# Kernel tuning notes

Measured on AMD Instinct MI355X. Metric: run time of the kernel, lower is better.

The kernel has to match this reference:

```python
import jax, jax.numpy as jnp
import numpy as np

N_ITEMS = 80001
D = 128
K = 20
HOP = 2
ROUTING_ITER = 4
SAMPLE = 12
B = 256
S = 50


def layer_norm(x, g, b, eps=1e-5):
    mu = jnp.mean(x, -1, keepdims=True)
    var = jnp.var(x, -1, keepdims=True)
    return (x - mu) * jax.lax.rsqrt(var + eps) * g + b


def routing_agg(x, nb0):
    # NeighborRoutingAgg (DisenGCN-style neighbor routing): x [N,d], nb0 [N,m] 0-based neighbor ids into x
    xn = x * jax.lax.rsqrt(jnp.sum(x * x, -1, keepdims=True) + 1e-12)
    z = xn[nb0]  # [N, m, d] irregular gather
    u = xn
    for _ in range(ROUTING_ITER):
        p = jax.nn.softmax(jnp.einsum('nd,nmd->nm', u, z), axis=1)
        u = xn + jnp.einsum('nm,nmd->nd', p, z)
        u = u * jax.lax.rsqrt(jnp.sum(u * u, -1, keepdims=True) + 1e-12)
    return u


def gru(x, W_ih, W_hh, b_ih, b_hh):
    # PyTorch nn.GRU, 1 layer, batch_first; x [B,S,d]
    Bb, Ss, d = x.shape
    h0 = jnp.zeros((Bb, d), x.dtype)
    gi_all = jnp.einsum('bsd,ed->bse', x, W_ih) + b_ih  # [B,S,3d] precompute input gates
    def step(h, gi):
        gh = h @ W_hh.T + b_hh
        i_r, i_z, i_n = jnp.split(gi, 3, -1)
        h_r, h_z, h_n = jnp.split(gh, 3, -1)
        r = jax.nn.sigmoid(i_r + h_r)
        zg = jax.nn.sigmoid(i_z + h_z)
        n = jnp.tanh(i_n + r * h_n)
        return (1.0 - zg) * n + zg * h, (1.0 - zg) * n + zg * h
    _, H = jax.lax.scan(step, h0, jnp.swapaxes(gi_all, 0, 1))
    return jnp.swapaxes(H, 0, 1)


def setup_inputs() -> dict:
    key = jax.random.key(0)
    ks = jax.random.split(key, 16)
    inp = {}
    inp['inp_sess'] = jax.random.randint(ks[0], (B, S), 0, N_ITEMS)
    inp['lengths'] = jax.random.randint(ks[1], (B,), 1, S + 1)
    inp['mask_inf'] = jnp.zeros((B, S), jnp.float32)
    inp['mask_1'] = jnp.ones((B, S), jnp.float32)
    inp['tau'] = jnp.float32(1.0)
    inp['adj_items'] = jax.random.randint(ks[2], (N_ITEMS, SAMPLE), 1, N_ITEMS)
    inp['anchors'] = jax.random.randint(ks[3], (K,), 1, N_ITEMS)
    inp['emb'] = jax.random.normal(ks[4], (N_ITEMS, D), jnp.float32) * 0.05
    inp['W_ih'] = jax.random.normal(ks[5], (3 * D, D), jnp.float32) * 0.05
    inp['W_hh'] = jax.random.normal(ks[6], (3 * D, D), jnp.float32) * 0.05
    inp['b_ih'] = jnp.zeros((3 * D,), jnp.float32)
    inp['b_hh'] = jnp.zeros((3 * D,), jnp.float32)
    inp['W1'] = jax.random.normal(ks[7], (D, D), jnp.float32) * 0.05
    inp['b1'] = jnp.zeros((D,), jnp.float32)
    inp['W2'] = jax.random.normal(ks[8], (K, D), jnp.float32) * 0.05
    inp['b2'] = jnp.zeros((K,), jnp.float32)
    inp['a1'] = jax.random.normal(ks[9], (1,), jnp.float32)
    inp['a2'] = jax.random.normal(ks[10], (1,), jnp.float32)
    for i, nm in enumerate(['ln1', 'ln2', 'ln3', 'ln4']):
        inp[nm + '_g'] = jnp.ones((D,), jnp.float32)
        inp[nm + '_b'] = jnp.zeros((D,), jnp.float32)
    return inp


def reference(inp_sess, lengths, mask_inf, mask_1, tau, adj_items, anchors, emb,
              W_ih, W_hh, b_ih, b_hh, W1, b1, W2, b2, a1, a2,
              ln1_g, ln1_b, ln2_g, ln2_b, ln3_g, ln3_b, ln4_g, ln4_b):
    # mask_inf / mask_1 are accepted by the torch forward but unused
    x = emb[1:]                       # [N-1, d] real items
    nb0 = adj_items[1:] - 1           # 0-based neighbor ids into x
    out = x
    acc = x
    for _ in range(HOP):
        out = routing_agg(out, nb0)
        acc = acc + out
    item_vectors = layer_norm(acc, ln1_g, ln1_b)          # [N-1, d]
    h = jax.nn.leaky_relu(item_vectors @ W1.T + b1)
    item_pop_prob = jax.nn.softmax((h @ W2.T + b2) / tau, axis=1)  # [N-1, K]
    anchors_emb = item_vectors[anchors - 1]               # [K, d]
    item_pop_vec = layer_norm(item_pop_prob @ anchors_emb, ln2_g, ln2_b)
    pad = jnp.zeros((1, D), item_vectors.dtype)
    iv = jnp.concatenate([pad, item_vectors], 0)          # [N, d]
    pv = jnp.concatenate([pad, item_pop_vec], 0)
    inp_emb = iv[inp_sess]                                # [B,S,d] (dropout off / eval)
    inp_pop = pv[inp_sess]
    H = layer_norm(gru(inp_emb, W_ih, W_hh, b_ih, b_hh), ln3_g, ln3_b)
    ht = H[jnp.arange(H.shape[0]), lengths - 1]           # [B, d]
    Hp = layer_norm(gru(inp_pop, W_ih, W_hh, b_ih, b_hh), ln4_g, ln4_b)
    ht_pop = Hp[jnp.arange(Hp.shape[0]), lengths - 1]
    scores_item = ht @ item_vectors.T                     # [B, N-1]
    scores_pop = ht_pop @ item_pop_vec.T
    scores = jax.nn.sigmoid(a1) * scores_item + jax.nn.sigmoid(a2) * scores_pop
    return scores, scores_item, scores_pop
```

## Files before the change

### kernel.cpp

```cpp
#include <hip/hip_runtime.h>

typedef unsigned short u16;
typedef unsigned int u32;
typedef __attribute__((ext_vector_type(8))) short short8;
typedef __attribute__((ext_vector_type(4))) float f32x4;

#define N_IT 80000
#define SLOT 10240000

__device__ __forceinline__ float wred(float v) {
#pragma unroll
    for (int s = 32; s; s >>= 1) v += __shfl_xor(v, s);
    return v;
}
__device__ __forceinline__ float sigf(float x) { return 1.f / (1.f + expf(-x)); }
__device__ __forceinline__ u16 f2bf(float f) {
    u32 x = __float_as_uint(f);
    u32 r = x + 0x7fffu + ((x >> 16) & 1u);
    return (u16)(r >> 16);
}
__device__ __forceinline__ float bf2f(u16 v) {
    return __uint_as_float(((u32)v) << 16);
}
__device__ __forceinline__ u32 pack2(float lo, float hi) {
    return ((u32)f2bf(hi) << 16) | f2bf(lo);
}
__device__ __forceinline__ f32x4 mfma16(short8 a, short8 b, f32x4 c) {
    return __builtin_amdgcn_mfma_f32_16x16x32_bf16(a, b, c, 0, 0, 0);
}
#define SWZ(v, pat) __int_as_float(__builtin_amdgcn_ds_swizzle(__float_as_int(v), pat))
__device__ __forceinline__ float red16(float t) {
    t += SWZ(t, 0x041F);
    t += SWZ(t, 0x081F);
    t += SWZ(t, 0x101F);
    t += SWZ(t, 0x201F);
    return t;
}
__device__ __forceinline__ float red16max(float t) {
    t = fmaxf(t, SWZ(t, 0x041F));
    t = fmaxf(t, SWZ(t, 0x081F));
    t = fmaxf(t, SWZ(t, 0x101F));
    t = fmaxf(t, SWZ(t, 0x201F));
    return t;
}
__device__ __forceinline__ float dot4(float4 a, float4 b) {
    return a.x * b.x + a.y * b.y + a.z * b.z + a.w * b.w;
}
__device__ __forceinline__ void unp8(uint4 w, float4& a, float4& b) {
    a.x = __uint_as_float(w.x << 16); a.y = __uint_as_float(w.x & 0xFFFF0000u);
    a.z = __uint_as_float(w.y << 16); a.w = __uint_as_float(w.y & 0xFFFF0000u);
    b.x = __uint_as_float(w.z << 16); b.y = __uint_as_float(w.z & 0xFFFF0000u);
    b.z = __uint_as_float(w.w << 16); b.w = __uint_as_float(w.w & 0xFFFF0000u);
}

__global__ __launch_bounds__(256) void k_cvtnorm(const float* __restrict__ Wih,
                                                 const float* __restrict__ W1,
                                                 const float* __restrict__ W2,
                                                 u16* __restrict__ wihbf,
                                                 u16* __restrict__ w1bf,
                                                 u16* __restrict__ w2bf,
                                                 const float* __restrict__ x,
                                                 u32* __restrict__ xn) {
    if (blockIdx.x < 272) {
        int i = blockIdx.x * 256 + threadIdx.x;
        if (i < 49152) {
            wihbf[i] = f2bf(Wih[i]);
        } else if (i < 65536) {
            int j = i - 49152;
            w1bf[j] = f2bf(W1[j]);
        } else if (i < 69632) {
            int j = i - 65536;
            int row = j >> 7, col = j & 127;
            w2bf[j] = (row < 20) ? f2bf(W2[row * 128 + col]) : (u16)0;
        }
        return;
    }
    int wid = ((blockIdx.x - 272) * 256 + threadIdx.x) >> 6;
    int l = threadIdx.x & 63;
    size_t base = (size_t)wid * 128;
    float2 v = *(const float2*)(x + base + 2 * l);
    float s = wred(v.x * v.x + v.y * v.y);
    float r = 1.f / sqrtf(s + 1e-12f);
    xn[(size_t)wid * 64 + l] = pack2(v.x * r, v.y * r);
}

__global__ __launch_bounds__(256, 2) void k_routeb(const u32* __restrict__ xn,
                                                   const int* __restrict__ adj,
                                                   u32* __restrict__ out) {
    int tid = blockIdx.x * 256 + threadIdx.x;
    int item = tid >> 4;
    int sl = threadIdx.x & 15;
    float4 x0, x1;
    unp8(*(const uint4*)(xn + (size_t)item * 64 + sl * 4), x0, x1);
    const int4* ar = (const int4*)(adj + (size_t)(item + 1) * 12);
    int4 a0 = ar[0], a1 = ar[1], a2 = ar[2];
    uint4 zw[12];
#define LDZ(i, comp) zw[i] = *(const uint4*)(xn + (size_t)((comp) - 1) * 64 + sl * 4);
    LDZ(0, a0.x) LDZ(1, a0.y) LDZ(2, a0.z) LDZ(3, a0.w)
    LDZ(4, a1.x) LDZ(5, a1.y) LDZ(6, a1.z) LDZ(7, a1.w)
    LDZ(8, a2.x) LDZ(9, a2.y) LDZ(10, a2.z) LDZ(11, a2.w)
#undef LDZ
    float4 u0 = x0, u1 = x1;
#pragma unroll
    for (int it = 0; it < 4; it++) {
        float p[12]; float sum = 0.f;
#pragma unroll
        for (int m = 0; m < 12; m++) {
            float4 a, b; unp8(zw[m], a, b);
            float t = dot4(u0, a) + dot4(u1, b);
            t = red16(t);
            p[m] = __expf(t);
            sum += p[m];
        }
        float inv = 1.f / sum;
        u0 = x0; u1 = x1;
#pragma unroll
        for (int m = 0; m < 12; m++) {
            float pm = p[m] * inv;
            float4 a, b; unp8(zw[m], a, b);
            u0.x += pm * a.x; u0.y += pm * a.y; u0.z += pm * a.z; u0.w += pm * a.w;
            u1.x += pm * b.x; u1.y += pm * b.y; u1.z += pm * b.z; u1.w += pm * b.w;
        }
        float nn = red16(dot4(u0, u0) + dot4(u1, u1));
        float rr = 1.f / sqrtf(nn + 1e-12f);
        u0.x *= rr; u0.y *= rr; u0.z *= rr; u0.w *= rr;
        u1.x *= rr; u1.y *= rr; u1.z *= rr; u1.w *= rr;
    }
    uint4 o = make_uint4(pack2(u0.x, u0.y), pack2(u0.z, u0.w),
                         pack2(u1.x, u1.y), pack2(u1.z, u1.w));
    *(uint4*)(out + (size_t)item * 64 + sl * 4) = o;
}

__global__ __launch_bounds__(256, 2) void k_route2lnb(const u32* __restrict__ xn,
                                                      const float* __restrict__ emb,
                                                      const int* __restrict__ adj,
                                                      const float* __restrict__ g,
                                                      const float* __restrict__ bb,
                                                      u32* __restrict__ ivbf) {
    int tid = blockIdx.x * 256 + threadIdx.x;
    int item = tid >> 4;
    int sl = threadIdx.x & 15;
    float4 x0, x1;
    unp8(*(const uint4*)(xn + (size_t)item * 64 + sl * 4), x0, x1);
    const int4* ar = (const int4*)(adj + (size_t)(item + 1) * 12);
    int4 a0 = ar[0], a1 = ar[1], a2 = ar[2];
    uint4 zw[12];
#define LDZ(i, comp) zw[i] = *(const uint4*)(xn + (size_t)((comp) - 1) * 64 + sl * 4);
    LDZ(0, a0.x) LDZ(1, a0.y) LDZ(2, a0.z) LDZ(3, a0.w)
    LDZ(4, a1.x) LDZ(5, a1.y) LDZ(6, a1.z) LDZ(7, a1.w)
    LDZ(8, a2.x) LDZ(9, a2.y) LDZ(10, a2.z) LDZ(11, a2.w)
#undef LDZ
    float4 u0 = x0, u1 = x1;
#pragma unroll
    for (int it = 0; it < 4; it++) {
        float p[12]; float sum = 0.f;
#pragma unroll
        for (int m = 0; m < 12; m++) {
            float4 a, b; unp8(zw[m], a, b);
            float t = dot4(u0, a) + dot4(u1, b);
            t = red16(t);
            p[m] = __expf(t);
            sum += p[m];
        }
        float inv = 1.f / sum;
        u0 = x0; u1 = x1;
#pragma unroll
        for (int m = 0; m < 12; m++) {
            float pm = p[m] * inv;
            float4 a, b; unp8(zw[m], a, b);
            u0.x += pm * a.x; u0.y += pm * a.y; u0.z += pm * a.z; u0.w += pm * a.w;
            u1.x += pm * b.x; u1.y += pm * b.y; u1.z += pm * b.z; u1.w += pm * b.w;
        }
        float nn = red16(dot4(u0, u0) + dot4(u1, u1));
        float rr = 1.f / sqrtf(nn + 1e-12f);
        u0.x *= rr; u0.y *= rr; u0.z *= rr; u0.w *= rr;
        u1.x *= rr; u1.y *= rr; u1.z *= rr; u1.w *= rr;
    }
    const float4* er = (const float4*)(emb + (size_t)item * 128 + sl * 8);
    float4 e0 = er[0], e1 = er[1];
    float v[8];
    v[0] = e0.x + x0.x + u0.x; v[1] = e0.y + x0.y + u0.y;
    v[2] = e0.z + x0.z + u0.z; v[3] = e0.w + x0.w + u0.w;
    v[4] = e1.x + x1.x + u1.x; v[5] = e1.y + x1.y + u1.y;
    v[6] = e1.z + x1.z + u1.z; v[7] = e1.w + x1.w + u1.w;
    float s = 0.f, q = 0.f;
#pragma unroll
    for (int j = 0; j < 8; j++) { s += v[j]; q += v[j] * v[j]; }
    s = red16(s); q = red16(q);
    float mean = s * (1.f / 128.f);
    float var = q * (1.f / 128.f) - mean * mean;
    float r = 1.f / sqrtf(var + 1e-5f);
    const float4* gr = (const float4*)(g + sl * 8);
    const float4* br = (const float4*)(bb + sl * 8);
    float4 g0 = gr[0], g1 = gr[1], bw0 = br[0], bw1 = br[1];
    float y[8];
    y[0] = (v[0] - mean) * r * g0.x + bw0.x; y[1] = (v[1] - mean) * r * g0.y + bw0.y;
    y[2] = (v[2] - mean) * r * g0.z + bw0.z; y[3] = (v[3] - mean) * r * g0.w + bw0.w;
    y[4] = (v[4] - mean) * r * g1.x + bw1.x; y[5] = (v[5] - mean) * r * g1.y + bw1.y;
    y[6] = (v[6] - mean) * r * g1.z + bw1.z; y[7] = (v[7] - mean) * r * g1.w + bw1.w;
    uint4 o = make_uint4(pack2(y[0], y[1]), pack2(y[2], y[3]),
                         pack2(y[4], y[5]), pack2(y[6], y[7]));
    *(uint4*)(ivbf + (size_t)item * 64 + sl * 4) = o;
}

__global__ __launch_bounds__(256, 2) void k_popm(const u16* __restrict__ ivbf,
                                                 const u16* __restrict__ w1bf,
                                                 const float* __restrict__ b1,
                                                 const u16* __restrict__ w2bf,
                                                 const float* __restrict__ b2,
                                                 const float* __restrict__ tau,
                                                 const int* __restrict__ anchors,
                                                 const float* __restrict__ g2,
                                                 const float* __restrict__ bb2,
                                                 u16* __restrict__ pvbf) {
    __shared__ u16 buf[4][16][136];
    __shared__ u16 anchS[128][40];
    int tid = threadIdx.x;
    for (int e = tid; e < 4096; e += 256) {
        int d = e >> 5, k = e & 31;
        anchS[d][k] = (k < 20) ? ivbf[(size_t)(anchors[k] - 1) * 128 + d] : (u16)0;
    }
    __syncthreads();
    int w = tid >> 6, l = tid & 63;
    int g16 = l >> 4, c = l & 15;
    int item0 = blockIdx.x * 64 + w * 16;
    const u16* ap = ivbf + (size_t)(item0 + c) * 128 + g16 * 8;
    short8 A[4];
#pragma unroll
    for (int kb = 0; kb < 4; kb++) A[kb] = *(const short8*)(ap + kb * 32);
#pragma unroll
    for (int nt = 0; nt < 8; nt++) {
        const u16* wp = w1bf + (nt * 16 + c) * 128 + g16 * 8;
        f32x4 acc = {0.f, 0.f, 0.f, 0.f};
#pragma unroll
        for (int kb = 0; kb < 4; kb++)
            acc = mfma16(A[kb], *(const short8*)(wp + kb * 32), acc);
        float bias = b1[nt * 16 + c];
#pragma unroll
        for (int qq = 0; qq < 4; qq++) {
            float hv = acc[qq] + bias;
            hv = hv >= 0.f ? hv : 0.01f * hv;
            buf[w][4 * g16 + qq][nt * 16 + c] = f2bf(hv);
        }
    }
    short8 A2[4];
#pragma unroll
    for (int kb = 0; kb < 4; kb++)
        A2[kb] = *(const short8*)&buf[w][c][g16 * 8 + kb * 32];
    f32x4 L0 = {0.f, 0.f, 0.f, 0.f}, L1 = {0.f, 0.f, 0.f, 0.f};
#pragma unroll
    for (int kb = 0; kb < 4; kb++) {
        L0 = mfma16(A2[kb], *(const short8*)(w2bf + c * 128 + g16 * 8 + kb * 32), L0);
        L1 = mfma16(A2[kb], *(const short8*)(w2bf + (16 + c) * 128 + g16 * 8 + kb * 32), L1);
    }
    float it = 1.f / tau[0];
    float b2v0 = b2[c];
    float b2v1 = (c < 4) ? b2[16 + c] : 0.f;
#pragma unroll
    for (int qq = 0; qq < 4; qq++) {
        float v0 = (L0[qq] + b2v0) * it;
        float v1 = (c < 4) ? (L1[qq] + b2v1) * it : -1e30f;
        float mx = red16max(fmaxf(v0, v1));
        float e0 = __expf(v0 - mx);
        float e1 = (c < 4) ? __expf(v1 - mx) : 0.f;
        float ssum = red16(e0 + e1);
        float inv = 1.f / ssum;
        buf[w][4 * g16 + qq][c] = f2bf(e0 * inv);
        buf[w][4 * g16 + qq][16 + c] = f2bf(e1 * inv);
    }
    short8 A3 = *(const short8*)&buf[w][c][g16 * 8];
    f32x4 pv[8];
#pragma unroll
    for (int nt = 0; nt < 8; nt++) {
        const short8 B3 = *(const short8*)&anchS[nt * 16 + c][g16 * 8];
        f32x4 zz = {0.f, 0.f, 0.f, 0.f};
        pv[nt] = mfma16(A3, B3, zz);
    }
    float g2v[8], b2gv[8];
#pragma unroll
    for (int t = 0; t < 8; t++) { g2v[t] = g2[t * 16 + c]; b2gv[t] = bb2[t * 16 + c]; }
#pragma unroll
    for (int qq = 0; qq < 4; qq++) {
        float ps = 0.f, psq = 0.f;
#pragma unroll
        for (int t = 0; t < 8; t++) { float x = pv[t][qq]; ps += x; psq += x * x; }
        float s = red16(ps), sq = red16(psq);
        float mean = s * (1.f / 128.f);
        float var = sq * (1.f / 128.f) - mean * mean;
        float r = 1.f / sqrtf(var + 1e-5f);
        size_t base = (size_t)(item0 + 4 * g16 + qq) * 128;
#pragma unroll
        for (int t = 0; t < 8; t++) {
            float y = (pv[t][qq] - mean) * r * g2v[t] + b2gv[t];
            pvbf[base + t * 16 + c] = f2bf(y);
        }
    }
}

__global__ __launch_bounds__(256) void k_gi(const int* __restrict__ sess,
                                            const u16* __restrict__ ivbf,
                                            const u16* __restrict__ pvbf,
                                            const u16* __restrict__ wbf,
                                            const float* __restrict__ bih,
                                            u16* __restrict__ gi) {
    int w = threadIdx.x >> 6, l = threadIdx.x & 63;
    int mt = blockIdx.x * 4 + w;
    int r = mt * 16 + (l & 15);
    int s = r / 50, t = r - s * 50;
    int idx = sess[(s & 255) * 50 + t];
    const u16* srcb = (s < 256) ? ivbf : pvbf;
    int ko = (l >> 4) * 8;
    const short8 Z8 = {0, 0, 0, 0, 0, 0, 0, 0};
    short8 A[4];
    if (idx == 0) {
#pragma unroll
        for (int kb = 0; kb < 4; kb++) A[kb] = Z8;
    } else {
        const u16* rp = srcb + (size_t)(idx - 1) * 128 + ko;
#pragma unroll
        for (int kb = 0; kb < 4; kb++) A[kb] = *(const short8*)(rp + kb * 32);
    }
    int rowb = mt * 16 + (l >> 4) * 4;
    for (int nt = 0; nt < 24; nt++) {
        int gcol = nt * 16 + (l & 15);
        const u16* wp = wbf + gcol * 128 + ko;
        f32x4 acc = {0.f, 0.f, 0.f, 0.f};
#pragma unroll
        for (int kb = 0; kb < 4; kb++)
            acc = mfma16(A[kb], *(const short8*)(wp + kb * 32), acc);
        float bias = bih[gcol];
#pragma unroll
        for (int q = 0; q < 4; q++)
            gi[(size_t)(rowb + q) * 384 + gcol] = f2bf(acc[q] + bias);
    }
}

__global__ __launch_bounds__(384, 2) void k_gru(const u16* __restrict__ gi,
                                                const float* __restrict__ whh,
                                                const float* __restrict__ bhh,
                                                const int* __restrict__ lengths,
                                                const float* __restrict__ g3,
                                                const float* __restrict__ b3,
                                                const float* __restrict__ g4,
                                                const float* __restrict__ b4,
                                                u32* __restrict__ htbf) {
    __shared__ __align__(16) float hS[2][128];
    __shared__ float rS[128], zS[128], hnS[128], inS[128];
    int g = threadIdx.x, b = blockIdx.x;
    float4 wv[32];
    const float4* wr = (const float4*)(whh + g * 128);
#pragma unroll
    for (int k = 0; k < 32; k++) wv[k] = wr[k];
    float bh = bhh[g];
    if (g < 128) hS[0][g] = 0.f;
    int len = lengths[b & 255];
    const u16* giS = gi + (size_t)b * 50 * 384 + g;
    __syncthreads();
    int par = 0;
    for (int t = 0; t < len; t++) {
        float ga = bf2f(giS[t * 384]);
        float aA = bh;
#pragma unroll
        for (int k = 0; k < 32; k++) {
            float4 w4 = wv[k];
            float4 ha = *(const float4*)&hS[par][k * 4];
            aA += w4.x * ha.x + w4.y * ha.y + w4.z * ha.z + w4.w * ha.w;
        }
        if (g < 128) {
            rS[g] = sigf(ga + aA);
        } else if (g < 256) {
            zS[g - 128] = sigf(ga + aA);
        } else {
            inS[g - 256] = ga; hnS[g - 256] = aA;
        }
        __syncthreads();
        if (g < 128) {
            float n = tanhf(inS[g] + rS[g] * hnS[g]);
            hS[par ^ 1][g] = (1.f - zS[g]) * n + zS[g] * hS[par][g];
        }
        __syncthreads();
        par ^= 1;
    }
    if (g < 64) {
        const float* lg = (b < 256) ? g3 : g4;
        const float* lb = (b < 256) ? b3 : b4;
        float2 v = *(const float2*)&hS[par][2 * g];
        float s = wred(v.x + v.y), q = wred(v.x * v.x + v.y * v.y);
        float mean = s * (1.f / 128.f), var = q * (1.f / 128.f) - mean * mean;
        float r = 1.f / sqrtf(var + 1e-5f);
        float2 gg = *(const float2*)(lg + 2 * g), bg = *(const float2*)(lb + 2 * g);
        float y0 = (v.x - mean) * r * gg.x + bg.x;
        float y1 = (v.y - mean) * r * gg.y + bg.y;
        htbf[(size_t)b * 64 + g] = ((u32)f2bf(y1) << 16) | f2bf(y0);
    }
}

__global__ __launch_bounds__(256) void k_scores(const u16* __restrict__ htbf,
                                                const u16* __restrict__ ivbf,
                                                const u16* __restrict__ pvbf,
                                                const float* __restrict__ a1,
                                                const float* __restrict__ a2,
                                                float* __restrict__ out) {
    int w = threadIdx.x >> 6, l = threadIdx.x & 63;
    int n0 = blockIdx.x * 64;
    int ko = (l >> 4) * 8;
    short8 Ai[4][4], Ap[4][4];
#pragma unroll
    for (int mi = 0; mi < 4; mi++) {
        int row = w * 64 + mi * 16 + (l & 15);
        const u16* pi = htbf + row * 128 + ko;
        const u16* pp = htbf + (row + 256) * 128 + ko;
#pragma unroll
        for (int kb = 0; kb < 4; kb++) {
            Ai[mi][kb] = *(const short8*)(pi + kb * 32);
            Ap[mi][kb] = *(const short8*)(pp + kb * 32);
        }
    }
    float s1 = sigf(a1[0]), s2 = sigf(a2[0]);
    float* sc = out;
    float* si = out + (size_t)20480000;
    float* sp = out + (size_t)40960000;
    for (int nt = 0; nt < 4; nt++) {
        int col = n0 + nt * 16 + (l & 15);
        const u16* bi = ivbf + (size_t)col * 128 + ko;
        const u16* bp = pvbf + (size_t)col * 128 + ko;
        short8 Bi[4], Bp[4];
#pragma unroll
        for (int kb = 0; kb < 4; kb++) {
            Bi[kb] = *(const short8*)(bi + kb * 32);
            Bp[kb] = *(const short8*)(bp + kb * 32);
        }
#pragma unroll
        for (int mi = 0; mi < 4; mi++) {
            f32x4 ai = {0.f, 0.f, 0.f, 0.f}, ap = {0.f, 0.f, 0.f, 0.f};
#pragma unroll
            for (int kb = 0; kb < 4; kb++) {
                ai = mfma16(Ai[mi][kb], Bi[kb], ai);
                ap = mfma16(Ap[mi][kb], Bp[kb], ap);
            }
            int rowb = w * 64 + mi * 16 + (l >> 4) * 4;
#pragma unroll
            for (int q = 0; q < 4; q++) {
                size_t o = (size_t)(rowb + q) * 80000 + col;
                float vi = ai[q], vp = ap[q];
                __builtin_nontemporal_store(vi, si + o);
                __builtin_nontemporal_store(vp, sp + o);
                __builtin_nontemporal_store(s1 * vi + s2 * vp, sc + o);
            }
        }
    }
}

extern "C" void kernel_launch(void* const* d_in, const int* in_sizes, int n_in,
                              void* d_out, int out_size, void* d_ws, size_t ws_size,
                              hipStream_t stream) {
    (void)in_sizes; (void)n_in; (void)out_size; (void)ws_size;
    const int*   sess    = (const int*)d_in[0];
    const int*   lengths = (const int*)d_in[1];
    const float* tau     = (const float*)d_in[4];
    const int*   adj     = (const int*)d_in[5];
    const int*   anchors = (const int*)d_in[6];
    const float* emb     = (const float*)d_in[7];
    const float* W_ih    = (const float*)d_in[8];
    const float* W_hh    = (const float*)d_in[9];
    const float* b_ih    = (const float*)d_in[10];
    const float* b_hh    = (const float*)d_in[11];
    const float* W1      = (const float*)d_in[12];
    const float* b1      = (const float*)d_in[13];
    const float* W2      = (const float*)d_in[14];
    const float* b2      = (const float*)d_in[15];
    const float* a1      = (const float*)d_in[16];
    const float* a2      = (const float*)d_in[17];
    const float* ln1g = (const float*)d_in[18];
    const float* ln1b = (const float*)d_in[19];
    const float* ln2g = (const float*)d_in[20];
    const float* ln2b = (const float*)d_in[21];
    const float* ln3g = (const float*)d_in[22];
    const float* ln3b = (const float*)d_in[23];
    const float* ln4g = (const float*)d_in[24];
    const float* ln4b = (const float*)d_in[25];

    float* out = (float*)d_out;
    u32* o_xn = (u32*)out;
    u32* o_o1 = (u32*)(out + SLOT);
    u16* o_gi = (u16*)(out + 2 * SLOT);

    u16* ws16   = (u16*)d_ws;
    u16* ivbf   = ws16;
    u16* pvbf   = ws16 + 10240000;
    u16* wihbf  = ws16 + 20480000;
    u16* htbf   = ws16 + 20529152;
    u16* w1bf   = ws16 + 20594688;
    u16* w2bf   = ws16 + 20611072;

    k_cvtnorm<<<20272, 256, 0, stream>>>(W_ih, W1, W2, wihbf, w1bf, w2bf,
                                         emb + 128, o_xn);
    k_routeb<<<5000, 256, 0, stream>>>(o_xn, adj, o_o1);
    k_route2lnb<<<5000, 256, 0, stream>>>(o_o1, emb + 128, adj, ln1g, ln1b, (u32*)ivbf);
    k_popm<<<1250, 256, 0, stream>>>(ivbf, w1bf, b1, w2bf, b2, tau, anchors,
                                     ln2g, ln2b, pvbf);
    k_gi<<<400, 256, 0, stream>>>(sess, ivbf, pvbf, wihbf, b_ih, o_gi);
    k_gru<<<512, 384, 0, stream>>>(o_gi, W_hh, b_hh, lengths, ln3g, ln3b, ln4g, ln4b,
                                   (u32*)htbf);
    k_scores<<<1250, 256, 0, stream>>>(htbf, ivbf, pvbf, a1, a2, out);
}
```

Measured before the change: 435.1 us.

## Batch 16 sequences per GRU block and compute recurrent matmul with bf16 MFMA

The GRU kernel now processes 16 sequences per block instead of one. W_hh is stored as swizzled bf16 in LDS, and each step's h·W_hh^T runs as MFMA tiles rather than per-thread fp32 dot products. The grid shrinks from 512 blocks to 32, so W_hh is loaded once per block, though far fewer CUs are busy. Each block now loops to the longest length among its 16 sequences and snapshots h at each sequence's last step. The recurrent state is rounded to bf16 and fast exp is used, which lowers precision.

```diff
diff --git a/kernel.cpp b/kernel.cpp
--- a/kernel.cpp
+++ b/kernel.cpp
@@ -335,7 +335,7 @@
     }
 }
 
-__global__ __launch_bounds__(384, 2) void k_gru(const u16* __restrict__ gi,
+__global__ __launch_bounds__(384, 1) void k_gru(const u16* __restrict__ gi,
                                                 const float* __restrict__ whh,
                                                 const float* __restrict__ bhh,
                                                 const int* __restrict__ lengths,
@@ -344,54 +344,75 @@
                                                 const float* __restrict__ g4,
                                                 const float* __restrict__ b4,
                                                 u32* __restrict__ htbf) {
-    __shared__ __align__(16) float hS[2][128];
-    __shared__ float rS[128], zS[128], hnS[128], inS[128];
-    int g = threadIdx.x, b = blockIdx.x;
-    float4 wv[32];
-    const float4* wr = (const float4*)(whh + g * 128);
-#pragma unroll
-    for (int k = 0; k < 32; k++) wv[k] = wr[k];
-    float bh = bhh[g];
-    if (g < 128) hS[0][g] = 0.f;
-    int len = lengths[b & 255];
-    const u16* giS = gi + (size_t)b * 50 * 384 + g;
+    __shared__ u16 whhS[49152];
+    __shared__ float gats[16][388];
+    __shared__ u16 hbfS[2048];
+    __shared__ float hfS[2048];
+    __shared__ float hsnapS[2048];
+    __shared__ float bhhS[384];
+    __shared__ int lenS[16];
+    int tid = threadIdx.x;
+    int sb = blockIdx.x * 16;
+    for (int e = tid; e < 49152; e += 384)
+        whhS[e ^ ((((u32)e >> 7) & 7) << 3)] = f2bf(whh[e]);
+    if (tid < 384) bhhS[tid] = bhh[tid];
+    if (tid < 16) lenS[tid] = lengths[(sb + tid) & 255];
+    for (int e = tid; e < 2048; e += 384) { hfS[e] = 0.f; hbfS[e] = 0; hsnapS[e] = 0.f; }
     __syncthreads();
-    int par = 0;
-    for (int t = 0; t < len; t++) {
-        float ga = bf2f(giS[t * 384]);
-        float aA = bh;
-#pragma unroll
-        for (int k = 0; k < 32; k++) {
-            float4 w4 = wv[k];
-            float4 ha = *(const float4*)&hS[par][k * 4];
-            aA += w4.x * ha.x + w4.y * ha.y + w4.z * ha.z + w4.w * ha.w;
-        }
-        if (g < 128) {
-            rS[g] = sigf(ga + aA);
-        } else if (g < 256) {
-            zS[g - 128] = sigf(ga + aA);
-        } else {
-            inS[g - 256] = ga; hnS[g - 256] = aA;
+    int lmax = 0;
+#pragma unroll
+    for (int i = 0; i < 16; i++) lmax = max(lmax, lenS[i]);
+    int w = tid >> 6, l = tid & 63;
+    int c16 = l & 15, hi = l >> 4, ko = hi * 8;
+    int aswz = (c16 & 7) << 3;
+    for (int t = 0; t < lmax; t++) {
+        short8 a[4];
+#pragma unroll
+        for (int kb = 0; kb < 4; kb++)
+            a[kb] = *(const short8*)&hbfS[(c16 * 128 + ko + kb * 32) ^ aswz];
+#pragma unroll
+        for (int ct = 0; ct < 4; ct++) {
+            int gcol = w * 64 + ct * 16 + c16;
+            int bswz = (gcol & 7) << 3;
+            f32x4 acc = {0.f, 0.f, 0.f, 0.f};
+#pragma unroll
+            for (int kb = 0; kb < 4; kb++)
+                acc = mfma16(a[kb],
+                             *(const short8*)&whhS[(gcol * 128 + ko + kb * 32) ^ bswz],
+                             acc);
+#pragma unroll
+            for (int q = 0; q < 4; q++) gats[hi * 4 + q][gcol] = acc[q];
         }
         __syncthreads();
-        if (g < 128) {
-            float n = tanhf(inS[g] + rS[g] * hnS[g]);
-            hS[par ^ 1][g] = (1.f - zS[g]) * n + zS[g] * hS[par][g];
+        for (int e = tid; e < 2048; e += 384) {
+            int s = e >> 7, d = e & 127;
+            size_t gb = ((size_t)(sb + s) * 50 + t) * 384;
+            float gr = bf2f(gi[gb + d]);
+            float gz = bf2f(gi[gb + 128 + d]);
+            float gn = bf2f(gi[gb + 256 + d]);
+            float r = 1.f / (1.f + __expf(-(gr + gats[s][d] + bhhS[d])));
+            float z = 1.f / (1.f + __expf(-(gz + gats[s][128 + d] + bhhS[128 + d])));
+            float narg = gn + r * (gats[s][256 + d] + bhhS[256 + d]);
+            float e2 = __expf(2.f * narg);
+            float n = 1.f - 2.f / (e2 + 1.f);
+            float hnew = (1.f - z) * n + z * hfS[e];
+            hfS[e] = hnew;
+            hbfS[e ^ ((s & 7) << 3)] = f2bf(hnew);
+            if (t == lenS[s] - 1) hsnapS[e] = hnew;
         }
         __syncthreads();
-        par ^= 1;
-    }
-    if (g < 64) {
-        const float* lg = (b < 256) ? g3 : g4;
-        const float* lb = (b < 256) ? b3 : b4;
-        float2 v = *(const float2*)&hS[par][2 * g];
-        float s = wred(v.x + v.y), q = wred(v.x * v.x + v.y * v.y);
-        float mean = s * (1.f / 128.f), var = q * (1.f / 128.f) - mean * mean;
+    }
+    const float* lg = (sb < 256) ? g3 : g4;
+    const float* lb = (sb < 256) ? b3 : b4;
+    for (int s = w; s < 16; s += 6) {
+        float2 v = *(const float2*)&hsnapS[s * 128 + 2 * l];
+        float su = wred(v.x + v.y), q = wred(v.x * v.x + v.y * v.y);
+        float mean = su * (1.f / 128.f), var = q * (1.f / 128.f) - mean * mean;
         float r = 1.f / sqrtf(var + 1e-5f);
-        float2 gg = *(const float2*)(lg + 2 * g), bg = *(const float2*)(lb + 2 * g);
+        float2 gg = *(const float2*)(lg + 2 * l), bg = *(const float2*)(lb + 2 * l);
         float y0 = (v.x - mean) * r * gg.x + bg.x;
         float y1 = (v.y - mean) * r * gg.y + bg.y;
-        htbf[(size_t)b * 64 + g] = ((u32)f2bf(y1) << 16) | f2bf(y0);
+        htbf[(size_t)(sb + s) * 64 + l] = pack2(y0, y1);
     }
 }
 
@@ -500,7 +521,7 @@
     k_popm<<<1250, 256, 0, stream>>>(ivbf, w1bf, b1, w2bf, b2, tau, anchors,
                                      ln2g, ln2b, pvbf);
     k_gi<<<400, 256, 0, stream>>>(sess, ivbf, pvbf, wihbf, b_ih, o_gi);
-    k_gru<<<512, 384, 0, stream>>>(o_gi, W_hh, b_hh, lengths, ln3g, ln3b, ln4g, ln4b,
-                                   (u32*)htbf);
+    k_gru<<<32, 384, 0, stream>>>(o_gi, W_hh, b_hh, lengths, ln3g, ln3b, ln4g, ln4b,
+                                  (u32*)htbf);
     k_scores<<<1250, 256, 0, stream>>>(htbf, ivbf, pvbf, a1, a2, out);
 }
```

Result: slower. 485.8 us (+11.6%).

## Batch item and pop GRU sequences per block with bf16 W_hh in LDS

Applied to the files above, without the earlier changes.

The GRU kernel now handles the item and popularity sequences of the same batch row in one block, so each W_hh row is read once for two recurrences. W_hh is converted to bf16 in the prep kernel and staged in XOR-swizzled shared memory instead of held in registers. The next timestep's input gates are prefetched, and sigmoid and tanh use fast exp. The grid is halved to 256 blocks at one block per SM, so the long serial recurrence runs on fewer CUs. The bf16 weights and fast intrinsics lower accuracy slightly.

```diff
diff --git a/kernel.cpp b/kernel.cpp
--- a/kernel.cpp
+++ b/kernel.cpp
@@ -56,12 +56,14 @@
 __global__ __launch_bounds__(256) void k_cvtnorm(const float* __restrict__ Wih,
                                                  const float* __restrict__ W1,
                                                  const float* __restrict__ W2,
+                                                 const float* __restrict__ Whh,
                                                  u16* __restrict__ wihbf,
                                                  u16* __restrict__ w1bf,
                                                  u16* __restrict__ w2bf,
+                                                 u16* __restrict__ whhbf,
                                                  const float* __restrict__ x,
                                                  u32* __restrict__ xn) {
-    if (blockIdx.x < 272) {
+    if (blockIdx.x < 464) {
         int i = blockIdx.x * 256 + threadIdx.x;
         if (i < 49152) {
             wihbf[i] = f2bf(Wih[i]);
@@ -72,10 +74,13 @@
             int j = i - 65536;
             int row = j >> 7, col = j & 127;
             w2bf[j] = (row < 20) ? f2bf(W2[row * 128 + col]) : (u16)0;
+        } else if (i < 118784) {
+            int j = i - 69632;
+            whhbf[j] = f2bf(Whh[j]);
         }
         return;
     }
-    int wid = ((blockIdx.x - 272) * 256 + threadIdx.x) >> 6;
+    int wid = ((blockIdx.x - 464) * 256 + threadIdx.x) >> 6;
     int l = threadIdx.x & 63;
     size_t base = (size_t)wid * 128;
     float2 v = *(const float2*)(x + base + 2 * l);
@@ -335,8 +340,8 @@
     }
 }
 
-__global__ __launch_bounds__(384, 2) void k_gru(const u16* __restrict__ gi,
-                                                const float* __restrict__ whh,
+__global__ __launch_bounds__(384, 1) void k_gru(const u16* __restrict__ gibf,
+                                                const u16* __restrict__ whhbf,
                                                 const float* __restrict__ bhh,
                                                 const int* __restrict__ lengths,
                                                 const float* __restrict__ g3,
@@ -344,54 +349,88 @@
                                                 const float* __restrict__ g4,
                                                 const float* __restrict__ b4,
                                                 u32* __restrict__ htbf) {
-    __shared__ __align__(16) float hS[2][128];
-    __shared__ float rS[128], zS[128], hnS[128], inS[128];
+    __shared__ u16 whhS[49152];
+    __shared__ __align__(16) float hA[2][128], hB[2][128];
+    __shared__ float rA[128], zA[128], hnA[128], inA[128];
+    __shared__ float rB[128], zB[128], hnB[128], inB[128];
     int g = threadIdx.x, b = blockIdx.x;
-    float4 wv[32];
-    const float4* wr = (const float4*)(whh + g * 128);
-#pragma unroll
-    for (int k = 0; k < 32; k++) wv[k] = wr[k];
+    for (int e8 = g * 8; e8 < 49152; e8 += 3072) {
+        uint4 v = *(const uint4*)&whhbf[e8];
+        *(uint4*)&whhS[e8 ^ (((e8 >> 7) & 15) << 3)] = v;
+    }
     float bh = bhh[g];
-    if (g < 128) hS[0][g] = 0.f;
-    int len = lengths[b & 255];
-    const u16* giS = gi + (size_t)b * 50 * 384 + g;
+    if (g < 128) { hA[0][g] = 0.f; hB[0][g] = 0.f; }
+    int len = lengths[b];
+    const u16* giA = gibf + (size_t)b * 50 * 384 + g;
+    const u16* giB = gibf + (size_t)(b + 256) * 50 * 384 + g;
+    int xo = (g & 15) << 3;
+    const u16* wrow = &whhS[g * 128];
+    float ga = bf2f(giA[0]), gb = bf2f(giB[0]);
     __syncthreads();
     int par = 0;
     for (int t = 0; t < len; t++) {
-        float ga = bf2f(giS[t * 384]);
-        float aA = bh;
-#pragma unroll
-        for (int k = 0; k < 32; k++) {
-            float4 w4 = wv[k];
-            float4 ha = *(const float4*)&hS[par][k * 4];
-            aA += w4.x * ha.x + w4.y * ha.y + w4.z * ha.z + w4.w * ha.w;
+        float ga_n = 0.f, gb_n = 0.f;
+        if (t + 1 < len) {
+            ga_n = bf2f(giA[(t + 1) * 384]);
+            gb_n = bf2f(giB[(t + 1) * 384]);
+        }
+        float aA = bh, aB = bh;
+#pragma unroll
+        for (int k = 0; k < 16; k++) {
+            uint4 wv = *(const uint4*)&wrow[(k * 8) ^ xo];
+            float4 w0, w1; unp8(wv, w0, w1);
+            const float4* hap = (const float4*)&hA[par][k * 8];
+            const float4* hbp = (const float4*)&hB[par][k * 8];
+            float4 ha0 = hap[0], ha1 = hap[1];
+            float4 hb0 = hbp[0], hb1 = hbp[1];
+            aA += dot4(w0, ha0) + dot4(w1, ha1);
+            aB += dot4(w0, hb0) + dot4(w1, hb1);
         }
         if (g < 128) {
-            rS[g] = sigf(ga + aA);
+            rA[g] = 1.f / (1.f + __expf(-(ga + aA)));
+            rB[g] = 1.f / (1.f + __expf(-(gb + aB)));
         } else if (g < 256) {
-            zS[g - 128] = sigf(ga + aA);
+            zA[g - 128] = 1.f / (1.f + __expf(-(ga + aA)));
+            zB[g - 128] = 1.f / (1.f + __expf(-(gb + aB)));
         } else {
-            inS[g - 256] = ga; hnS[g - 256] = aA;
+            inA[g - 256] = ga; hnA[g - 256] = aA;
+            inB[g - 256] = gb; hnB[g - 256] = aB;
         }
         __syncthreads();
         if (g < 128) {
-            float n = tanhf(inS[g] + rS[g] * hnS[g]);
-            hS[par ^ 1][g] = (1.f - zS[g]) * n + zS[g] * hS[par][g];
+            float narg = inA[g] + rA[g] * hnA[g];
+            float e2 = __expf(2.f * narg);
+            float n = 1.f - 2.f / (e2 + 1.f);
+            hA[par ^ 1][g] = (1.f - zA[g]) * n + zA[g] * hA[par][g];
+        } else if (g < 256) {
+            int d = g - 128;
+            float narg = inB[d] + rB[d] * hnB[d];
+            float e2 = __expf(2.f * narg);
+            float n = 1.f - 2.f / (e2 + 1.f);
+            hB[par ^ 1][d] = (1.f - zB[d]) * n + zB[d] * hB[par][d];
         }
         __syncthreads();
-        par ^= 1;
-    }
-    if (g < 64) {
-        const float* lg = (b < 256) ? g3 : g4;
-        const float* lb = (b < 256) ? b3 : b4;
-        float2 v = *(const float2*)&hS[par][2 * g];
+        par ^= 1; ga = ga_n; gb = gb_n;
+    }
+    int w = g >> 6, l = g & 63;
+    if (w == 0) {
+        float2 v = *(const float2*)&hA[par][2 * l];
         float s = wred(v.x + v.y), q = wred(v.x * v.x + v.y * v.y);
         float mean = s * (1.f / 128.f), var = q * (1.f / 128.f) - mean * mean;
         float r = 1.f / sqrtf(var + 1e-5f);
-        float2 gg = *(const float2*)(lg + 2 * g), bg = *(const float2*)(lb + 2 * g);
+        float2 gg = *(const float2*)(g3 + 2 * l), bg = *(const float2*)(b3 + 2 * l);
         float y0 = (v.x - mean) * r * gg.x + bg.x;
         float y1 = (v.y - mean) * r * gg.y + bg.y;
-        htbf[(size_t)b * 64 + g] = ((u32)f2bf(y1) << 16) | f2bf(y0);
+        htbf[(size_t)b * 64 + l] = pack2(y0, y1);
+    } else if (w == 1) {
+        float2 v = *(const float2*)&hB[par][2 * l];
+        float s = wred(v.x + v.y), q = wred(v.x * v.x + v.y * v.y);
+        float mean = s * (1.f / 128.f), var = q * (1.f / 128.f) - mean * mean;
+        float r = 1.f / sqrtf(var + 1e-5f);
+        float2 gg = *(const float2*)(g4 + 2 * l), bg = *(const float2*)(b4 + 2 * l);
+        float y0 = (v.x - mean) * r * gg.x + bg.x;
+        float y1 = (v.y - mean) * r * gg.y + bg.y;
+        htbf[(size_t)(b + 256) * 64 + l] = pack2(y0, y1);
     }
 }
 
@@ -492,15 +531,16 @@
     u16* htbf   = ws16 + 20529152;
     u16* w1bf   = ws16 + 20594688;
     u16* w2bf   = ws16 + 20611072;
-
-    k_cvtnorm<<<20272, 256, 0, stream>>>(W_ih, W1, W2, wihbf, w1bf, w2bf,
-                                         emb + 128, o_xn);
+    u16* whhbf  = ws16 + 20615168;
+
+    k_cvtnorm<<<20464, 256, 0, stream>>>(W_ih, W1, W2, W_hh, wihbf, w1bf, w2bf,
+                                         whhbf, emb + 128, o_xn);
     k_routeb<<<5000, 256, 0, stream>>>(o_xn, adj, o_o1);
     k_route2lnb<<<5000, 256, 0, stream>>>(o_o1, emb + 128, adj, ln1g, ln1b, (u32*)ivbf);
     k_popm<<<1250, 256, 0, stream>>>(ivbf, w1bf, b1, w2bf, b2, tau, anchors,
                                      ln2g, ln2b, pvbf);
     k_gi<<<400, 256, 0, stream>>>(sess, ivbf, pvbf, wihbf, b_ih, o_gi);
-    k_gru<<<512, 384, 0, stream>>>(o_gi, W_hh, b_hh, lengths, ln3g, ln3b, ln4g, ln4b,
+    k_gru<<<256, 384, 0, stream>>>(o_gi, whhbf, b_hh, lengths, ln3g, ln3b, ln4g, ln4b,
                                    (u32*)htbf);
     k_scores<<<1250, 256, 0, stream>>>(htbf, ivbf, pvbf, a1, a2, out);
 }
```

After: 413.4 us. -5.0%, faster.
